# Kernel optimization log

Hardware: AMD Instinct MI355X
Metric: run time of the kernel (lower is better)

The kernel has to match this reference:

```python
import jax, jax.numpy as jnp
import numpy as np

D_MODEL, D_STATE, D_CONV, EXPAND = 1024, 16, 4, 2
D_INNER = EXPAND * D_MODEL            # 2048
DT_RANK = (D_MODEL + 15) // 16        # 64 (mamba 'auto')
B, L = 2, 2048
EPS = 1e-5


def setup_inputs() -> dict:
    key = jax.random.key(0)
    ks = jax.random.split(key, 12)
    s = lambda k, shape, sc=0.02: jax.random.normal(k, shape, dtype=jnp.float32) * sc
    return {
        "x": jax.random.normal(ks[0], (B, L, D_MODEL), dtype=jnp.float32),
        "ln_w": jnp.ones((D_MODEL,), jnp.float32),
        "ln_b": jnp.zeros((D_MODEL,), jnp.float32),
        "W_in": s(ks[1], (2 * D_INNER, D_MODEL)),
        "conv_w": s(ks[2], (D_INNER, D_CONV), 0.2),
        "conv_b": jnp.zeros((D_INNER,), jnp.float32),
        "W_xproj": s(ks[3], (DT_RANK + 2 * D_STATE, D_INNER)),
        "W_dt": s(ks[4], (D_INNER, DT_RANK), 0.1),
        "b_dt": jax.random.uniform(ks[5], (D_INNER,), jnp.float32, -4.0, -2.0),  # softplus(b)~dt_min
        "A_log": jnp.log(jnp.broadcast_to(jnp.arange(1, D_STATE + 1, dtype=jnp.float32), (D_INNER, D_STATE))),
        "D": jnp.ones((D_INNER,), jnp.float32),
        "W_out": s(ks[6], (D_MODEL, D_INNER)),
    }


def _mamba_forward(x, ln_w, ln_b, W_in, conv_w, conv_b, W_xproj, W_dt, b_dt, A_log, D, W_out):
    # Pre-norm LayerNorm
    mu = jnp.mean(x, axis=-1, keepdims=True)
    var = jnp.mean(jnp.square(x - mu), axis=-1, keepdims=True)
    xn = (x - mu) * jax.lax.rsqrt(var + EPS) * ln_w + ln_b

    # in_proj -> [B, L, 2*d_inner]; split into x-branch and gate z
    xz = jnp.einsum("bld,ed->ble", xn, W_in)
    u, z = jnp.split(xz, 2, axis=-1)

    # causal depthwise conv1d over L, kernel width D_CONV
    u_pad = jnp.pad(u, ((0, 0), (D_CONV - 1, 0), (0, 0)))
    uc = conv_b[None, None, :]
    for k in range(D_CONV):
        uc = uc + u_pad[:, k:k + L, :] * conv_w[:, k]
    u = jax.nn.silu(uc)  # [B, L, d_inner]

    # input-dependent dt, B, C
    dbl = jnp.einsum("bld,ed->ble", u, W_xproj)
    dt_r = dbl[..., :DT_RANK]
    Bm = dbl[..., DT_RANK:DT_RANK + D_STATE]          # [B, L, n]
    Cm = dbl[..., DT_RANK + D_STATE:]                 # [B, L, n]
    dt = jax.nn.softplus(jnp.einsum("blr,dr->bld", dt_r, W_dt) + b_dt)  # [B, L, d]

    A = -jnp.exp(A_log)  # [d, n]

    # selective scan over L; carry h: [B, d, n]
    def step(h, inp):
        dt_t, B_t, C_t, u_t = inp  # [B,d], [B,n], [B,n], [B,d]
        dA = jnp.exp(dt_t[:, :, None] * A[None])                 # [B, d, n]
        h = dA * h + (dt_t * u_t)[:, :, None] * B_t[:, None, :]  # [B, d, n]
        y_t = jnp.einsum("bdn,bn->bd", h, C_t)
        return h, y_t

    xs = (jnp.moveaxis(dt, 1, 0), jnp.moveaxis(Bm, 1, 0),
          jnp.moveaxis(Cm, 1, 0), jnp.moveaxis(u, 1, 0))
    h0 = jnp.zeros((x.shape[0], D_INNER, D_STATE), x.dtype)
    _, ys = jax.lax.scan(step, h0, xs)
    y = jnp.moveaxis(ys, 0, 1) + u * D  # [B, L, d_inner]

    y = y * jax.nn.silu(z)
    out = jnp.einsum("bld,ed->ble", y, W_out)
    return x + out


def reference(x, ln_w, ln_b, W_in, conv_w, conv_b, W_xproj, W_dt, b_dt, A_log, D, W_out):
    return _mamba_forward(x, ln_w, ln_b, W_in, conv_w, conv_b, W_xproj, W_dt, b_dt, A_log, D, W_out)
```

## Files before the change

kernel.cpp:

```cpp
#include <hip/hip_runtime.h>
#include <hip/hip_bf16.h>
#include <stdint.h>

typedef __hip_bfloat16 bf16;
typedef __attribute__((ext_vector_type(8))) short short8;
typedef __attribute__((ext_vector_type(4))) short short4v;
typedef __attribute__((ext_vector_type(4))) float floatx4;

#define D_MODEL 1024
#define D_STATE 16
#define D_INNER 2048
#define DT_RANK 64
#define BB 2
#define LL 2048
#define BL (BB * LL)
#define XZ_LD (2 * D_INNER)
#define DBL_LD (DT_RANK + 2 * D_STATE)
#define NCH 64
#define TCH (LL / NCH)

__device__ __forceinline__ bf16 f2b(float f) { return __float2bfloat16(f); }

__device__ __forceinline__ float fsig(float v)  { return __fdividef(1.f, 1.f + __expf(-v)); }
__device__ __forceinline__ float fsoftp(float v){ return fmaxf(v, 0.f) + __logf(1.f + __expf(-fabsf(v))); }

__device__ __forceinline__ void gload16(const void* g, void* l) {
    __builtin_amdgcn_global_load_lds(
        (const __attribute__((address_space(1))) uint32_t*)(uintptr_t)g,
        (__attribute__((address_space(3))) uint32_t*)(uintptr_t)l,
        16, 0, 0);
}

#define S0 (4096 * 1024)
#define S1 (128 * 2048)
#define S2 (2048 * 64)
#define S3 (1024 * 2048)
#define S4 (BL * DBL_LD)
#define WCVT_TOT (S0 + S1 + S2 + S3 + S4)

__global__ __launch_bounds__(256) void prep_kernel(
    const float* __restrict__ x, const float* __restrict__ w,
    const float* __restrict__ b, bf16* __restrict__ xnb,
    const float* __restrict__ Win, const float* __restrict__ Wx,
    const float* __restrict__ Wdt, const float* __restrict__ Wout,
    bf16* __restrict__ win_bf, bf16* __restrict__ wx_bf,
    bf16* __restrict__ wdt_bf, bf16* __restrict__ wout_bf,
    float* __restrict__ dbl)
{
    __shared__ float s1[256], s2[256];
    const int tid = threadIdx.x;
    if (blockIdx.x < BL) {
        const int row = blockIdx.x;
        const float* xr = x + (size_t)row * D_MODEL;
        float v[4], sum = 0.f, sq = 0.f;
#pragma unroll
        for (int i = 0; i < 4; ++i) {
            v[i] = xr[tid + 256 * i];
            sum += v[i];
            sq  += v[i] * v[i];
        }
        s1[tid] = sum; s2[tid] = sq;
        __syncthreads();
        for (int s = 128; s > 0; s >>= 1) {
            if (tid < s) { s1[tid] += s1[tid + s]; s2[tid] += s2[tid + s]; }
            __syncthreads();
        }
        const float mu  = s1[0] * (1.f / D_MODEL);
        const float var = s2[0] * (1.f / D_MODEL) - mu * mu;
        const float rs  = rsqrtf(var + 1e-5f);
#pragma unroll
        for (int i = 0; i < 4; ++i) {
            const int c = tid + 256 * i;
            xnb[(size_t)row * D_MODEL + c] = f2b((v[i] - mu) * rs * w[c] + b[c]);
        }
    } else {
        int id = (blockIdx.x - BL) * 256 + tid;
        if (id < S0) { win_bf[id] = f2b(Win[id]); return; }
        id -= S0;
        if (id < S1) { wx_bf[id] = (id < 96 * 2048) ? f2b(Wx[id]) : f2b(0.f); return; }
        id -= S1;
        if (id < S2) { wdt_bf[id] = f2b(Wdt[id]); return; }
        id -= S2;
        if (id < S3) { wout_bf[id] = f2b(Wout[id]); return; }
        id -= S3;
        dbl[id] = 0.f;
    }
}

#define GTM 128
#define GTN 128
#define GTK 32

template <int EPI>
__global__ __launch_bounds__(256) void gemm_t(
    const bf16* __restrict__ A, int lda,
    const bf16* __restrict__ B, int ldb,
    float* __restrict__ C, int ldc,
    int N, int K,
    const float* __restrict__ bias,
    bf16* __restrict__ C2)
{
    __shared__ short As[GTM * GTK];
    __shared__ short Bs[GTN * GTK];
    const int tid  = threadIdx.x;
    const int lane = tid & 63;
    const int wave = tid >> 6;
    const int wm = (wave & 1) * 64;
    const int wn = (wave >> 1) * 64;
    const int bm = blockIdx.y * GTM;
    const int bn = blockIdx.x * GTN;
    const int kbase = blockIdx.z * K;

    floatx4 acc[4][4];
#pragma unroll
    for (int i = 0; i < 4; ++i)
#pragma unroll
        for (int j = 0; j < 4; ++j) acc[i][j] = (floatx4){0.f, 0.f, 0.f, 0.f};

    const int srow = wave * 16 + (lane >> 2);
    const int scol = (lane & 3) * 8;
    const int fm = lane & 15;
    const int q  = lane >> 4;

    for (int k0 = 0; k0 < K; k0 += GTK) {
#pragma unroll
        for (int r = 0; r < 2; ++r) {
            const int m = r * 64 + srow;
            gload16(A + (size_t)(bm + m) * lda + kbase + k0 + scol,
                    As + m * GTK + scol);
            gload16(B + (size_t)(bn + m) * ldb + kbase + k0 + scol,
                    Bs + m * GTK + scol);
        }
        __syncthreads();

        short8 af[4], bfr[4];
#pragma unroll
        for (int i = 0; i < 4; ++i)
            af[i] = *(short8*)&As[(wm + i * 16 + fm) * GTK + q * 8];
#pragma unroll
        for (int j = 0; j < 4; ++j)
            bfr[j] = *(short8*)&Bs[(wn + j * 16 + fm) * GTK + q * 8];
#pragma unroll
        for (int i = 0; i < 4; ++i)
#pragma unroll
            for (int j = 0; j < 4; ++j)
                acc[i][j] = __builtin_amdgcn_mfma_f32_16x16x32_bf16(
                    af[i], bfr[j], acc[i][j], 0, 0, 0);
        __syncthreads();
    }

    const int col = lane & 15;
    const int rq  = (lane >> 4) * 4;
#pragma unroll
    for (int i = 0; i < 4; ++i) {
#pragma unroll
        for (int j = 0; j < 4; ++j) {
#pragma unroll
            for (int r = 0; r < 4; ++r) {
                const int gm = bm + wm + i * 16 + rq + r;
                const int gn = bn + wn + j * 16 + col;
                if (gn >= N) continue;
                float v = acc[i][j][r];
                if constexpr (EPI == 3) {
                    atomicAdd(&C[(size_t)gm * ldc + gn], v);
                } else if constexpr (EPI == 4) {
                    if (gn < D_INNER) C[(size_t)gm * ldc + gn] = v;
                    else C2[(size_t)gm * (size_t)D_INNER + (gn - D_INNER)] = f2b(v);
                } else {
                    C2[(size_t)gm * ldc + gn] = f2b(fsoftp(v + bias[gn]));
                }
            }
        }
    }
}

#define PNT (D_MODEL / 64)

__global__ __launch_bounds__(512, 2) void gemm256_uz(
    const bf16* __restrict__ A,
    const bf16* __restrict__ B,
    float* __restrict__ U,
    bf16* __restrict__ Z)
{
    __shared__ __attribute__((aligned(16))) short lds[65536];
    const int t    = threadIdx.x;
    const int lane = t & 63;
    const int wid  = t >> 6;
    const int wm   = wid >> 2;
    const int wn   = wid & 3;
    const int fm   = lane & 15;
    const int q    = lane >> 4;

    const int lin = (int)blockIdx.x;
    const int nid = (lin & 7) * 32 + (lin >> 3);
    const int bm  = (nid >> 4) * 256;
    const int bn  = (nid & 15) * 256;

    const int sg   = (((t & 7) ^ ((t >> 3) & 7)) << 3);
    const int ldst = t * 8;
    const short* Agp = (const short*)A + (size_t)(bm + (t >> 3)) * D_MODEL + sg;
    const short* Bgp = (const short*)B + (size_t)(bn + (t >> 3)) * D_MODEL + sg;

#define STG(g, lb) do { \
        gload16((g),                           &lds[(lb) + ldst]);        \
        gload16((g) + (size_t)64 * D_MODEL,    &lds[(lb) + 4096 + ldst]); \
    } while (0)

    const int ss0 = ((q ^ (fm & 7)) << 3);
    const int ss1 = (((4 + q) ^ (fm & 7)) << 3);
    const int aro = fm * 64;
    const int bro = ((wn & 1) * 64 + fm) * 64;

    floatx4 acc[8][4];
#pragma unroll
    for (int i = 0; i < 8; ++i)
#pragma unroll
        for (int j = 0; j < 4; ++j) acc[i][j] = (floatx4){0.f, 0.f, 0.f, 0.f};

    STG(Agp, 0);
    STG(Agp + (size_t)128 * D_MODEL, 8192);
    STG(Bgp, 32768);
    STG(Bgp + (size_t)128 * D_MODEL, 32768 + 8192);

    for (int kt = 0; kt < PNT; ++kt) {
        const int d = kt & 1;
        if (kt + 1 < PNT) {
            const int kn = (kt + 1) * 64;
            const int nb = (d ^ 1) * 16384;
            STG(Agp + kn,                         nb);
            STG(Agp + (size_t)128 * D_MODEL + kn, nb + 8192);
            STG(Bgp + kn,                         32768 + nb);
            STG(Bgp + (size_t)128 * D_MODEL + kn, 32768 + nb + 8192);
            asm volatile("s_waitcnt vmcnt(8)" ::: "memory");
        } else {
            asm volatile("s_waitcnt vmcnt(0)" ::: "memory");
        }
        __builtin_amdgcn_s_barrier();

        const short* Ab = &lds[d * 16384 + wm * 8192];
        const short* Bb = &lds[32768 + d * 16384 + (wn >> 1) * 8192];

        short8 bfr[4][2];
#pragma unroll
        for (int cf = 0; cf < 4; ++cf) {
            bfr[cf][0] = *(const short8*)(Bb + bro + cf * 1024 + ss0);
            bfr[cf][1] = *(const short8*)(Bb + bro + cf * 1024 + ss1);
        }

#pragma unroll
        for (int qd = 0; qd < 4; ++qd) {
            short8 af[2][2];
#pragma unroll
            for (int i = 0; i < 2; ++i) {
                af[i][0] = *(const short8*)(Ab + (qd * 2 + i) * 1024 + aro + ss0);
                af[i][1] = *(const short8*)(Ab + (qd * 2 + i) * 1024 + aro + ss1);
            }
            __builtin_amdgcn_s_barrier();
            __builtin_amdgcn_s_setprio(1);
#pragma unroll
            for (int i = 0; i < 2; ++i)
#pragma unroll
                for (int cf = 0; cf < 4; ++cf) {
                    acc[qd * 2 + i][cf] = __builtin_amdgcn_mfma_f32_16x16x32_bf16(
                        af[i][0], bfr[cf][0], acc[qd * 2 + i][cf], 0, 0, 0);
                    acc[qd * 2 + i][cf] = __builtin_amdgcn_mfma_f32_16x16x32_bf16(
                        af[i][1], bfr[cf][1], acc[qd * 2 + i][cf], 0, 0, 0);
                }
            __builtin_amdgcn_s_setprio(0);
            __builtin_amdgcn_s_barrier();
        }
    }
#undef STG

    const int gm0 = bm + wm * 128 + q * 4;
    const int gn0 = bn + wn * 64 + fm;
    if (bn < D_INNER) {
#pragma unroll
        for (int rf = 0; rf < 8; ++rf)
#pragma unroll
            for (int cf = 0; cf < 4; ++cf)
#pragma unroll
                for (int r = 0; r < 4; ++r)
                    U[(size_t)(gm0 + rf * 16 + r) * D_INNER + gn0 + cf * 16] =
                        acc[rf][cf][r];
    } else {
#pragma unroll
        for (int rf = 0; rf < 8; ++rf)
#pragma unroll
            for (int cf = 0; cf < 4; ++cf)
#pragma unroll
                for (int r = 0; r < 4; ++r)
                    Z[(size_t)(gm0 + rf * 16 + r) * D_INNER + gn0 + cf * 16 - D_INNER] =
                        f2b(acc[rf][cf][r]);
    }
}

#define ONT (D_INNER / 64)

__global__ __launch_bounds__(512, 2) void gemm_out8(
    const bf16* __restrict__ A,
    const bf16* __restrict__ B,
    const float* __restrict__ resid,
    float* __restrict__ C)
{
    __shared__ __attribute__((aligned(16))) short lds[32768];
    const int t    = threadIdx.x;
    const int lane = t & 63;
    const int wid  = t >> 6;
    const int wm   = wid >> 2;
    const int wn   = wid & 3;
    const int fm   = lane & 15;
    const int q    = lane >> 4;

    const int lin = (int)blockIdx.x;
    const int nid = (lin & 7) * 32 + (lin >> 3);
    const int bm  = (nid >> 3) * 128;
    const int bn  = (nid & 7) * 128;

    const int sg   = (((t & 7) ^ ((t >> 3) & 7)) << 3);
    const int ldst = t * 8;
    const short* Agp = (const short*)A + (size_t)(bm + (t >> 3)) * D_INNER + sg;
    const short* Bgp = (const short*)B + (size_t)(bn + (t >> 3)) * D_INNER + sg;

#define OSTG(g, lb) do { \
        gload16((g),                        &lds[(lb) + ldst]);        \
        gload16((g) + (size_t)64 * D_INNER, &lds[(lb) + 4096 + ldst]); \
    } while (0)

    const int ss0 = ((q ^ (fm & 7)) << 3);
    const int ss1 = (((4 + q) ^ (fm & 7)) << 3);
    const int fro = fm * 64;

    floatx4 acc[4][2];
#pragma unroll
    for (int i = 0; i < 4; ++i)
#pragma unroll
        for (int j = 0; j < 2; ++j) acc[i][j] = (floatx4){0.f, 0.f, 0.f, 0.f};

    OSTG(Agp, 0);
    OSTG(Bgp, 16384);

    for (int kt = 0; kt < ONT; ++kt) {
        const int d = kt & 1;
        if (kt + 1 < ONT) {
            const int kn = (kt + 1) * 64;
            const int nb = (d ^ 1) * 8192;
            OSTG(Agp + kn, nb);
            OSTG(Bgp + kn, 16384 + nb);
            asm volatile("s_waitcnt vmcnt(4)" ::: "memory");
        } else {
            asm volatile("s_waitcnt vmcnt(0)" ::: "memory");
        }
        __builtin_amdgcn_s_barrier();

        const short* Ab = &lds[d * 8192 + wm * 4096];
        const short* Bb = &lds[16384 + d * 8192 + wn * 2048];

        short8 bfr[2][2];
#pragma unroll
        for (int cf = 0; cf < 2; ++cf) {
            bfr[cf][0] = *(const short8*)(Bb + cf * 1024 + fro + ss0);
            bfr[cf][1] = *(const short8*)(Bb + cf * 1024 + fro + ss1);
        }

#pragma unroll
        for (int qd = 0; qd < 2; ++qd) {
            short8 af[2][2];
#pragma unroll
            for (int i = 0; i < 2; ++i) {
                af[i][0] = *(const short8*)(Ab + (qd * 2 + i) * 1024 + fro + ss0);
                af[i][1] = *(const short8*)(Ab + (qd * 2 + i) * 1024 + fro + ss1);
            }
            __builtin_amdgcn_s_barrier();
            __builtin_amdgcn_s_setprio(1);
#pragma unroll
            for (int i = 0; i < 2; ++i)
#pragma unroll
                for (int cf = 0; cf < 2; ++cf) {
                    acc[qd * 2 + i][cf] = __builtin_amdgcn_mfma_f32_16x16x32_bf16(
                        af[i][0], bfr[cf][0], acc[qd * 2 + i][cf], 0, 0, 0);
                    acc[qd * 2 + i][cf] = __builtin_amdgcn_mfma_f32_16x16x32_bf16(
                        af[i][1], bfr[cf][1], acc[qd * 2 + i][cf], 0, 0, 0);
                }
            __builtin_amdgcn_s_setprio(0);
            __builtin_amdgcn_s_barrier();
        }
    }
#undef OSTG

    const int gm0 = bm + wm * 64 + q * 4;
    const int gn0 = bn + wn * 32 + fm;
#pragma unroll
    for (int i = 0; i < 4; ++i)
#pragma unroll
        for (int cf = 0; cf < 2; ++cf)
#pragma unroll
            for (int r = 0; r < 4; ++r) {
                const size_t idx = (size_t)(gm0 + i * 16 + r) * D_MODEL + gn0 + cf * 16;
                C[idx] = acc[i][cf][r] + resid[idx];
            }
}

#define CCH 128
#define CTC (LL / CCH)

__global__ __launch_bounds__(256) void conv_v2(
    const float* __restrict__ uraw, const float* __restrict__ cw,
    const float* __restrict__ cb, bf16* __restrict__ ucb)
{
    const int blk = blockIdx.x;
    const int c  = blk & (CCH - 1);
    const int dg = (blk >> 7) & 1;
    const int b  = blk >> 8;
    const int d4 = dg * 1024 + threadIdx.x * 4;
    float w0[4], w1[4], w2[4], w3[4], bias[4];
#pragma unroll
    for (int j = 0; j < 4; ++j) {
        bias[j] = cb[d4 + j];
        w0[j] = cw[(d4 + j) * 4 + 0];
        w1[j] = cw[(d4 + j) * 4 + 1];
        w2[j] = cw[(d4 + j) * 4 + 2];
        w3[j] = cw[(d4 + j) * 4 + 3];
    }
    const size_t base = ((size_t)b * LL + (size_t)c * CTC) * D_INNER + d4;
    floatx4 x0 = {0.f, 0.f, 0.f, 0.f}, x1 = x0, x2 = x0;
    if (c > 0) {
        x0 = *(const floatx4*)(uraw + base - 3 * (size_t)D_INNER);
        x1 = *(const floatx4*)(uraw + base - 2 * (size_t)D_INNER);
        x2 = *(const floatx4*)(uraw + base - 1 * (size_t)D_INNER);
    }
#pragma unroll
    for (int tt = 0; tt < CTC; ++tt) {
        const floatx4 x3 = *(const floatx4*)(uraw + base + (size_t)tt * D_INNER);
        short4v o;
#pragma unroll
        for (int j = 0; j < 4; ++j) {
            float a = bias[j] + x0[j] * w0[j] + x1[j] * w1[j]
                              + x2[j] * w2[j] + x3[j] * w3[j];
            a = a * fsig(a);
            bf16 h = f2b(a);
            unsigned short us;
            __builtin_memcpy(&us, &h, 2);
            o[j] = (short)us;
        }
        *(short4v*)(ucb + base + (size_t)tt * D_INNER) = o;
        x0 = x1; x1 = x2; x2 = x3;
    }
}

__global__ __launch_bounds__(256) void cvt_dtr(
    const float* __restrict__ dbl, bf16* __restrict__ dtr_bf)
{
    const int id = blockIdx.x * 256 + threadIdx.x;
    const int m = id >> 6, r = id & 63;
    dtr_bf[id] = f2b(dbl[(size_t)m * DBL_LD + r]);
}

__global__ __launch_bounds__(256) void scan_p1(
    const bf16* __restrict__ uc, const bf16* __restrict__ dtb,
    const float* __restrict__ dbl, const float* __restrict__ A_log,
    float* __restrict__ Psum, float* __restrict__ Hloc)
{
    const int blk = blockIdx.x;
    const int d = (blk & 7) * 256 + threadIdx.x;
    const int c = (blk >> 3) & (NCH - 1);
    const int b = blk >> 9;
    float A[D_STATE], h[D_STATE];
    bool lin = true;
#pragma unroll
    for (int n = 0; n < D_STATE; ++n) {
        A[n] = -__expf(A_log[d * D_STATE + n]);
        lin = lin && (fabsf(A[n] + (float)(n + 1)) < 1e-3f);
        h[n] = 0.f;
    }
    const size_t row0 = (size_t)b * LL + c * TCH;
    const bf16* dtp = dtb + row0 * D_INNER + d;
    const bf16* up  = uc  + row0 * D_INNER + d;
    const float* Bp = dbl + row0 * DBL_LD + DT_RANK;
    float S = 0.f;
    if (lin) {
        for (int t = 0; t < TCH; ++t) {
            const float dtv = (float)dtp[(size_t)t * D_INNER];
            const float uv  = (float)up[(size_t)t * D_INNER];
            const float du  = dtv * uv;
            S += dtv;
            const float e1 = __expf(-dtv);
            float dA = 1.f;
#pragma unroll
            for (int n = 0; n < D_STATE; ++n) {
                dA *= e1;
                h[n] = dA * h[n] + du * Bp[(size_t)t * DBL_LD + n];
            }
        }
    } else {
        for (int t = 0; t < TCH; ++t) {
            const float dtv = (float)dtp[(size_t)t * D_INNER];
            const float uv  = (float)up[(size_t)t * D_INNER];
            const float du  = dtv * uv;
            S += dtv;
#pragma unroll
            for (int n = 0; n < D_STATE; ++n)
                h[n] = __expf(dtv * A[n]) * h[n] + du * Bp[(size_t)t * DBL_LD + n];
        }
    }
    const size_t o = (((size_t)b * NCH + c) * D_INNER + d) * D_STATE;
    if (lin) {
        const float E1 = __expf(-S);
        float P = 1.f;
#pragma unroll
        for (int n = 0; n < D_STATE; ++n) {
            P *= E1;
            Psum[o + n] = P;
            Hloc[o + n] = h[n];
        }
    } else {
#pragma unroll
        for (int n = 0; n < D_STATE; ++n) {
            Psum[o + n] = __expf(S * A[n]);
            Hloc[o + n] = h[n];
        }
    }
}

__global__ __launch_bounds__(256) void scan_p2(
    float* __restrict__ Psum, const float* __restrict__ Hloc)
{
    const int id = blockIdx.x * 256 + threadIdx.x;
    const int dn = id & (D_INNER * D_STATE - 1);
    const int b  = id >> 15;
    float h = 0.f;
    for (int c = 0; c < NCH; ++c) {
        const size_t o = ((size_t)(b * NCH + c) * D_INNER * D_STATE) + dn;
        const float P  = Psum[o];
        const float hl = Hloc[o];
        Psum[o] = h;
        h = P * h + hl;
    }
}

__global__ __launch_bounds__(256) void scan_p3b(
    bf16* __restrict__ ucy, const bf16* __restrict__ dtb,
    const float* __restrict__ dbl, const float* __restrict__ A_log,
    const float* __restrict__ Dw, const float* __restrict__ Hin,
    const bf16* __restrict__ zbf)
{
    const int blk = blockIdx.x;
    const int d = (blk & 7) * 256 + threadIdx.x;
    const int c = (blk >> 3) & (NCH - 1);
    const int b = blk >> 9;
    float A[D_STATE], h[D_STATE];
    const size_t o = (((size_t)b * NCH + c) * D_INNER + d) * D_STATE;
    bool lin = true;
#pragma unroll
    for (int n = 0; n < D_STATE; ++n) {
        A[n] = -__expf(A_log[d * D_STATE + n]);
        lin = lin && (fabsf(A[n] + (float)(n + 1)) < 1e-3f);
        h[n] = Hin[o + n];
    }
    const float Dd = Dw[d];
    const size_t row0 = (size_t)b * LL + c * TCH;
    const bf16* dtp = dtb + row0 * D_INNER + d;
    bf16*       uyp = ucy + row0 * D_INNER + d;
    const float* BCp = dbl + row0 * DBL_LD;
    const bf16* zp   = zbf + row0 * D_INNER + d;
    if (lin) {
        for (int t = 0; t < TCH; ++t) {
            const float dtv = (float)dtp[(size_t)t * D_INNER];
            const float uv  = (float)uyp[(size_t)t * D_INNER];
            const float du  = dtv * uv;
            float acc = uv * Dd;
            const float* Brow = BCp + (size_t)t * DBL_LD + DT_RANK;
            const float* Crow = Brow + D_STATE;
            const float e1 = __expf(-dtv);
            float dA = 1.f;
#pragma unroll
            for (int n = 0; n < D_STATE; ++n) {
                dA *= e1;
                h[n] = dA * h[n] + du * Brow[n];
                acc += h[n] * Crow[n];
            }
            const float zv = (float)zp[(size_t)t * D_INNER];
            uyp[(size_t)t * D_INNER] = f2b(acc * zv * fsig(zv));
        }
    } else {
        for (int t = 0; t < TCH; ++t) {
            const float dtv = (float)dtp[(size_t)t * D_INNER];
            const float uv  = (float)uyp[(size_t)t * D_INNER];
            const float du  = dtv * uv;
            float acc = uv * Dd;
            const float* Brow = BCp + (size_t)t * DBL_LD + DT_RANK;
            const float* Crow = Brow + D_STATE;
#pragma unroll
            for (int n = 0; n < D_STATE; ++n) {
                h[n] = __expf(dtv * A[n]) * h[n] + du * Brow[n];
                acc += h[n] * Crow[n];
            }
            const float zv = (float)zp[(size_t)t * D_INNER];
            uyp[(size_t)t * D_INNER] = f2b(acc * zv * fsig(zv));
        }
    }
}

#define BM 128
#define BN 128
#define BK 8

__global__ __launch_bounds__(256) void ln_kernel(
    const float* __restrict__ x, const float* __restrict__ w,
    const float* __restrict__ b, float* __restrict__ xnf)
{
    __shared__ float s1[256], s2[256];
    const int row = blockIdx.x;
    const int tid = threadIdx.x;
    const float* xr = x + (size_t)row * D_MODEL;
    float v[4], sum = 0.f, sq = 0.f;
#pragma unroll
    for (int i = 0; i < 4; ++i) {
        v[i] = xr[tid + 256 * i];
        sum += v[i];
        sq  += v[i] * v[i];
    }
    s1[tid] = sum; s2[tid] = sq;
    __syncthreads();
    for (int s = 128; s > 0; s >>= 1) {
        if (tid < s) { s1[tid] += s1[tid + s]; s2[tid] += s2[tid + s]; }
        __syncthreads();
    }
    const float mu  = s1[0] * (1.f / D_MODEL);
    const float var = s2[0] * (1.f / D_MODEL) - mu * mu;
    const float rs  = rsqrtf(var + 1e-5f);
#pragma unroll
    for (int i = 0; i < 4; ++i) {
        const int c = tid + 256 * i;
        xnf[(size_t)row * D_MODEL + c] = (v[i] - mu) * rs * w[c] + b[c];
    }
}

__global__ __launch_bounds__(256) void gemm_bt(
    const float* __restrict__ A, int lda,
    const float* __restrict__ Bw,
    float* __restrict__ C, int ldc,
    int M, int N, int K, int epi,
    const float* __restrict__ bias,
    const float* __restrict__ resid)
{
    __shared__ float As[BK][BM + 1];
    __shared__ float Bs[BK][BN + 1];
    const int tx = threadIdx.x, ty = threadIdx.y;
    const int tid = ty * 16 + tx;
    const int bm = blockIdx.y * BM, bn = blockIdx.x * BN;
    float acc[8][8];
#pragma unroll
    for (int i = 0; i < 8; ++i)
#pragma unroll
        for (int j = 0; j < 8; ++j) acc[i][j] = 0.f;
    for (int k0 = 0; k0 < K; k0 += BK) {
#pragma unroll
        for (int i = tid; i < BM * BK; i += 256) {
            const int m = i / BK, kk = i % BK;
            As[kk][m] = A[(size_t)(bm + m) * lda + (k0 + kk)];
        }
#pragma unroll
        for (int i = tid; i < BN * BK; i += 256) {
            const int n = i / BK, kk = i % BK;
            const int gn = bn + n;
            Bs[kk][n] = (gn < N) ? Bw[(size_t)gn * K + (k0 + kk)] : 0.f;
        }
        __syncthreads();
#pragma unroll
        for (int kk = 0; kk < BK; ++kk) {
            float av[8], bv[8];
#pragma unroll
            for (int i = 0; i < 8; ++i) av[i] = As[kk][ty * 8 + i];
#pragma unroll
            for (int j = 0; j < 8; ++j) bv[j] = Bs[kk][tx * 8 + j];
#pragma unroll
            for (int i = 0; i < 8; ++i)
#pragma unroll
                for (int j = 0; j < 8; ++j) acc[i][j] += av[i] * bv[j];
        }
        __syncthreads();
    }
#pragma unroll
    for (int i = 0; i < 8; ++i) {
        const int gm = bm + ty * 8 + i;
#pragma unroll
        for (int j = 0; j < 8; ++j) {
            const int gn = bn + tx * 8 + j;
            if (gn >= N) continue;
            float v = acc[i][j];
            if (epi == 1) {
                v += bias[gn];
                v = fmaxf(v, 0.f) + log1pf(expf(-fabsf(v)));
            } else if (epi == 2) {
                v += resid[(size_t)gm * ldc + gn];
            }
            C[(size_t)gm * ldc + gn] = v;
        }
    }
}

__global__ __launch_bounds__(256) void conv_silu_kernel(
    float* __restrict__ xz, const float* __restrict__ cw,
    const float* __restrict__ cb)
{
    const int idx = blockIdx.x * 256 + threadIdx.x;
    const int b = idx >> 11, d = idx & (D_INNER - 1);
    const float w0 = cw[d * 4 + 0], w1 = cw[d * 4 + 1];
    const float w2 = cw[d * 4 + 2], w3 = cw[d * 4 + 3];
    const float bias = cb[d];
    float* u = xz + (size_t)b * LL * XZ_LD + d;
    float x0 = 0.f, x1 = 0.f, x2 = 0.f;
    for (int t = 0; t < LL; ++t) {
        const float x3 = u[(size_t)t * XZ_LD];
        const float c = bias + x0 * w0 + x1 * w1 + x2 * w2 + x3 * w3;
        u[(size_t)t * XZ_LD] = c / (1.f + expf(-c));
        x0 = x1; x1 = x2; x2 = x3;
    }
}

__global__ __launch_bounds__(256) void scan_kernel(
    float* __restrict__ xz, const float* __restrict__ dtb,
    const float* __restrict__ dbl,
    const float* __restrict__ A_log, const float* __restrict__ Dw)
{
    const int idx = blockIdx.x * 256 + threadIdx.x;
    const int b = idx >> 11, d = idx & (D_INNER - 1);
    float A[D_STATE], h[D_STATE];
#pragma unroll
    for (int n = 0; n < D_STATE; ++n) {
        A[n] = -expf(A_log[d * D_STATE + n]);
        h[n] = 0.f;
    }
    const float Dd = Dw[d];
    const float* dtp  = dtb + (size_t)b * LL * D_INNER + d;
    float*       up   = xz  + (size_t)b * LL * XZ_LD + d;
    const float* dblp = dbl + (size_t)b * LL * DBL_LD;
    for (int t = 0; t < LL; ++t) {
        const float dtv = dtp[(size_t)t * D_INNER];
        const float uv  = up[(size_t)t * XZ_LD];
        const float zv  = up[(size_t)t * XZ_LD + D_INNER];
        const float* Brow = dblp + (size_t)t * DBL_LD + DT_RANK;
        const float* Crow = Brow + D_STATE;
        const float du = dtv * uv;
        float acc = uv * Dd;
#pragma unroll
        for (int n = 0; n < D_STATE; ++n) {
            const float dA = expf(dtv * A[n]);
            h[n] = dA * h[n] + du * Brow[n];
            acc += h[n] * Crow[n];
        }
        const float sz = zv / (1.f + expf(-zv));
        up[(size_t)t * XZ_LD] = acc * sz;
    }
}

extern "C" void kernel_launch(void* const* d_in, const int* in_sizes, int n_in,
                              void* d_out, int out_size, void* d_ws, size_t ws_size,
                              hipStream_t stream)
{
    const float* x       = (const float*)d_in[0];
    const float* ln_w    = (const float*)d_in[1];
    const float* ln_b    = (const float*)d_in[2];
    const float* W_in    = (const float*)d_in[3];
    const float* conv_w  = (const float*)d_in[4];
    const float* conv_b  = (const float*)d_in[5];
    const float* W_xproj = (const float*)d_in[6];
    const float* W_dt    = (const float*)d_in[7];
    const float* b_dt    = (const float*)d_in[8];
    const float* A_log   = (const float*)d_in[9];
    const float* Dw      = (const float*)d_in[10];
    const float* W_out   = (const float*)d_in[11];
    float* out = (float*)d_out;

    float* wsf     = (float*)d_ws;
    bf16*  dtb_bf  = (bf16*)wsf;
    float* uraw    = wsf + 4194304;
    bf16*  zbf     = (bf16*)(wsf + 12582912);
    float* Psum    = wsf + 16777216;
    float* Hloc    = wsf + 20971520;
    float* dbl     = wsf + 25165824;
    bf16*  ucy     = (bf16*)(wsf + 25559040);
    bf16*  xn_bf   = (bf16*)(wsf + 29753344);
    bf16*  win_bf  = (bf16*)(wsf + 31850496);
    bf16*  wx_bf   = (bf16*)(wsf + 33947648);
    bf16*  wdt_bf  = (bf16*)(wsf + 34078720);
    bf16*  wout_bf = (bf16*)(wsf + 34144256);
    bf16*  dtr_bf  = (bf16*)(wsf + 35192832);
    const size_t need_big = (size_t)35323904 * sizeof(float);

    if (ws_size >= need_big) {
        prep_kernel<<<BL + WCVT_TOT / 256, 256, 0, stream>>>(
            x, ln_w, ln_b, xn_bf,
            W_in, W_xproj, W_dt, W_out, win_bf, wx_bf, wdt_bf, wout_bf, dbl);
        gemm256_uz<<<dim3(256), 512, 0, stream>>>(xn_bf, win_bf, uraw, zbf);
        conv_v2<<<BB * 2 * CCH, 256, 0, stream>>>(uraw, conv_w, conv_b, ucy);
        gemm_t<3><<<dim3(1, BL / GTM, 8), 256, 0, stream>>>(
            ucy, D_INNER, wx_bf, D_INNER, dbl, DBL_LD,
            DBL_LD, D_INNER / 8, nullptr, nullptr);
        cvt_dtr<<<BL * DT_RANK / 256, 256, 0, stream>>>(dbl, dtr_bf);
        gemm_t<5><<<dim3(D_INNER / GTN, BL / GTM, 1), 256, 0, stream>>>(
            dtr_bf, DT_RANK, wdt_bf, DT_RANK, nullptr, D_INNER,
            D_INNER, DT_RANK, b_dt, dtb_bf);
        scan_p1<<<BB * NCH * 8, 256, 0, stream>>>(
            ucy, dtb_bf, dbl, A_log, Psum, Hloc);
        scan_p2<<<BB * D_INNER * D_STATE / 256, 256, 0, stream>>>(Psum, Hloc);
        scan_p3b<<<BB * NCH * 8, 256, 0, stream>>>(
            ucy, dtb_bf, dbl, A_log, Dw, Psum, zbf);
        gemm_out8<<<dim3(256), 512, 0, stream>>>(ucy, wout_bf, x, out);
    } else {
        float* fdtb = wsf;
        float* fxn  = fdtb;
        float* fxz  = fdtb + (size_t)BL * D_INNER;
        float* fdbl = fxz + (size_t)BL * XZ_LD;
        ln_kernel<<<BL, 256, 0, stream>>>(x, ln_w, ln_b, fxn);
        dim3 blk(16, 16);
        gemm_bt<<<dim3(XZ_LD / BN, BL / BM), blk, 0, stream>>>(
            fxn, D_MODEL, W_in, fxz, XZ_LD, BL, XZ_LD, D_MODEL, 0, nullptr, nullptr);
        conv_silu_kernel<<<(BB * D_INNER) / 256, 256, 0, stream>>>(fxz, conv_w, conv_b);
        gemm_bt<<<dim3(1, BL / BM), blk, 0, stream>>>(
            fxz, XZ_LD, W_xproj, fdbl, DBL_LD, BL, DBL_LD, D_INNER, 0, nullptr, nullptr);
        gemm_bt<<<dim3(D_INNER / BN, BL / BM), blk, 0, stream>>>(
            fdbl, DBL_LD, W_dt, fdtb, D_INNER, BL, D_INNER, DT_RANK, 1, b_dt, nullptr);
        scan_kernel<<<(BB * D_INNER) / 256, 256, 0, stream>>>(fxz, fdtb, fdbl, A_log, Dw);
        gemm_bt<<<dim3(D_MODEL / BN, BL / BM), blk, 0, stream>>>(
            fxz, XZ_LD, W_out, out, D_MODEL, BL, D_MODEL, D_INNER, 2, nullptr, x);
    }
}
```

Baseline: 284.5 us.

## Shrink in_proj GEMM tiles to 128 and replace split-K atomics with partial-sum reduction

The in_proj GEMM moves from 256x256 tiles (256 blocks) to 128x128 tiles (1024 blocks) with half the LDS, giving more blocks to spread across CUs at the cost of less per-tile reuse. The x_proj split-K GEMM now writes per-split partial sums into a scratch buffer (reusing the uraw region) instead of doing atomicAdd into dbl. A new reduction kernel sums the 8 partials and writes both dbl and the bf16 dt_rank slice, which replaces the separate cvt_dtr kernel. This removes atomic contention and the pre-zeroing dependency on dbl, but adds an extra pass over the partial buffer.

```diff
diff --git a/kernel.cpp b/kernel.cpp
--- a/kernel.cpp
+++ b/kernel.cpp
@@ -161,11 +161,8 @@
                 const int gn = bn + wn + j * 16 + col;
                 if (gn >= N) continue;
                 float v = acc[i][j][r];
-                if constexpr (EPI == 3) {
-                    atomicAdd(&C[(size_t)gm * ldc + gn], v);
-                } else if constexpr (EPI == 4) {
-                    if (gn < D_INNER) C[(size_t)gm * ldc + gn] = v;
-                    else C2[(size_t)gm * (size_t)D_INNER + (gn - D_INNER)] = f2b(v);
+                if constexpr (EPI == 6) {
+                    C[((size_t)blockIdx.z * BL + gm) * 128 + gn] = v;
                 } else {
                     C2[(size_t)gm * ldc + gn] = f2b(fsoftp(v + bias[gn]));
                 }
@@ -174,15 +171,29 @@
     }
 }
 
-#define PNT (D_MODEL / 64)
-
-__global__ __launch_bounds__(512, 2) void gemm256_uz(
+__global__ __launch_bounds__(256) void red_dbl(
+    const float* __restrict__ P, float* __restrict__ dbl,
+    bf16* __restrict__ dtr_bf)
+{
+    const int id = blockIdx.x * 256 + threadIdx.x;
+    const int n = id & 127, m = id >> 7;
+    if (n >= DBL_LD) return;
+    float s = 0.f;
+#pragma unroll
+    for (int k = 0; k < 8; ++k) s += P[(size_t)k * BL * 128 + id];
+    dbl[(size_t)m * DBL_LD + n] = s;
+    if (n < DT_RANK) dtr_bf[(size_t)m * DT_RANK + n] = f2b(s);
+}
+
+#define GNT (D_MODEL / 64)
+
+__global__ __launch_bounds__(512, 2) void gemm128_uz(
     const bf16* __restrict__ A,
     const bf16* __restrict__ B,
     float* __restrict__ U,
     bf16* __restrict__ Z)
 {
-    __shared__ __attribute__((aligned(16))) short lds[65536];
+    __shared__ __attribute__((aligned(16))) short lds[32768];
     const int t    = threadIdx.x;
     const int lane = t & 63;
     const int wid  = t >> 6;
@@ -192,75 +203,70 @@
     const int q    = lane >> 4;
 
     const int lin = (int)blockIdx.x;
-    const int nid = (lin & 7) * 32 + (lin >> 3);
-    const int bm  = (nid >> 4) * 256;
-    const int bn  = (nid & 15) * 256;
+    const int nid = (lin & 7) * 128 + (lin >> 3);
+    const int bm  = (nid >> 5) * 128;
+    const int bn  = (nid & 31) * 128;
 
     const int sg   = (((t & 7) ^ ((t >> 3) & 7)) << 3);
     const int ldst = t * 8;
     const short* Agp = (const short*)A + (size_t)(bm + (t >> 3)) * D_MODEL + sg;
     const short* Bgp = (const short*)B + (size_t)(bn + (t >> 3)) * D_MODEL + sg;
 
-#define STG(g, lb) do { \
-        gload16((g),                           &lds[(lb) + ldst]);        \
-        gload16((g) + (size_t)64 * D_MODEL,    &lds[(lb) + 4096 + ldst]); \
+#define GSTG(g, lb) do { \
+        gload16((g),                        &lds[(lb) + ldst]);        \
+        gload16((g) + (size_t)64 * D_MODEL, &lds[(lb) + 4096 + ldst]); \
     } while (0)
 
     const int ss0 = ((q ^ (fm & 7)) << 3);
     const int ss1 = (((4 + q) ^ (fm & 7)) << 3);
-    const int aro = fm * 64;
-    const int bro = ((wn & 1) * 64 + fm) * 64;
-
-    floatx4 acc[8][4];
-#pragma unroll
-    for (int i = 0; i < 8; ++i)
-#pragma unroll
-        for (int j = 0; j < 4; ++j) acc[i][j] = (floatx4){0.f, 0.f, 0.f, 0.f};
-
-    STG(Agp, 0);
-    STG(Agp + (size_t)128 * D_MODEL, 8192);
-    STG(Bgp, 32768);
-    STG(Bgp + (size_t)128 * D_MODEL, 32768 + 8192);
-
-    for (int kt = 0; kt < PNT; ++kt) {
+    const int fro = fm * 64;
+
+    floatx4 acc[4][2];
+#pragma unroll
+    for (int i = 0; i < 4; ++i)
+#pragma unroll
+        for (int j = 0; j < 2; ++j) acc[i][j] = (floatx4){0.f, 0.f, 0.f, 0.f};
+
+    GSTG(Agp, 0);
+    GSTG(Bgp, 16384);
+
+    for (int kt = 0; kt < GNT; ++kt) {
         const int d = kt & 1;
-        if (kt + 1 < PNT) {
+        if (kt + 1 < GNT) {
             const int kn = (kt + 1) * 64;
-            const int nb = (d ^ 1) * 16384;
-            STG(Agp + kn,                         nb);
-            STG(Agp + (size_t)128 * D_MODEL + kn, nb + 8192);
-            STG(Bgp + kn,                         32768 + nb);
-            STG(Bgp + (size_t)128 * D_MODEL + kn, 32768 + nb + 8192);
-            asm volatile("s_waitcnt vmcnt(8)" ::: "memory");
+            const int nb = (d ^ 1) * 8192;
+            GSTG(Agp + kn, nb);
+            GSTG(Bgp + kn, 16384 + nb);
+            asm volatile("s_waitcnt vmcnt(4)" ::: "memory");
         } else {
             asm volatile("s_waitcnt vmcnt(0)" ::: "memory");
         }
         __builtin_amdgcn_s_barrier();
 
-        const short* Ab = &lds[d * 16384 + wm * 8192];
-        const short* Bb = &lds[32768 + d * 16384 + (wn >> 1) * 8192];
-
-        short8 bfr[4][2];
-#pragma unroll
-        for (int cf = 0; cf < 4; ++cf) {
-            bfr[cf][0] = *(const short8*)(Bb + bro + cf * 1024 + ss0);
-            bfr[cf][1] = *(const short8*)(Bb + bro + cf * 1024 + ss1);
-        }
-
-#pragma unroll
-        for (int qd = 0; qd < 4; ++qd) {
+        const short* Ab = &lds[d * 8192 + wm * 4096];
+        const short* Bb = &lds[16384 + d * 8192 + wn * 2048];
+
+        short8 bfr[2][2];
+#pragma unroll
+        for (int cf = 0; cf < 2; ++cf) {
+            bfr[cf][0] = *(const short8*)(Bb + cf * 1024 + fro + ss0);
+            bfr[cf][1] = *(const short8*)(Bb + cf * 1024 + fro + ss1);
+        }
+
+#pragma unroll
+        for (int qd = 0; qd < 2; ++qd) {
             short8 af[2][2];
 #pragma unroll
             for (int i = 0; i < 2; ++i) {
-                af[i][0] = *(const short8*)(Ab + (qd * 2 + i) * 1024 + aro + ss0);
-                af[i][1] = *(const short8*)(Ab + (qd * 2 + i) * 1024 + aro + ss1);
+                af[i][0] = *(const short8*)(Ab + (qd * 2 + i) * 1024 + fro + ss0);
+                af[i][1] = *(const short8*)(Ab + (qd * 2 + i) * 1024 + fro + ss1);
             }
             __builtin_amdgcn_s_barrier();
             __builtin_amdgcn_s_setprio(1);
 #pragma unroll
             for (int i = 0; i < 2; ++i)
 #pragma unroll
-                for (int cf = 0; cf < 4; ++cf) {
+                for (int cf = 0; cf < 2; ++cf) {
                     acc[qd * 2 + i][cf] = __builtin_amdgcn_mfma_f32_16x16x32_bf16(
                         af[i][0], bfr[cf][0], acc[qd * 2 + i][cf], 0, 0, 0);
                     acc[qd * 2 + i][cf] = __builtin_amdgcn_mfma_f32_16x16x32_bf16(
@@ -270,28 +276,28 @@
             __builtin_amdgcn_s_barrier();
         }
     }
-#undef STG
-
-    const int gm0 = bm + wm * 128 + q * 4;
-    const int gn0 = bn + wn * 64 + fm;
+#undef GSTG
+
+    const int gm0 = bm + wm * 64 + q * 4;
+    const int gn0 = bn + wn * 32 + fm;
     if (bn < D_INNER) {
 #pragma unroll
-        for (int rf = 0; rf < 8; ++rf)
-#pragma unroll
-            for (int cf = 0; cf < 4; ++cf)
+        for (int i = 0; i < 4; ++i)
+#pragma unroll
+            for (int cf = 0; cf < 2; ++cf)
 #pragma unroll
                 for (int r = 0; r < 4; ++r)
-                    U[(size_t)(gm0 + rf * 16 + r) * D_INNER + gn0 + cf * 16] =
-                        acc[rf][cf][r];
+                    U[(size_t)(gm0 + i * 16 + r) * D_INNER + gn0 + cf * 16] =
+                        acc[i][cf][r];
     } else {
 #pragma unroll
-        for (int rf = 0; rf < 8; ++rf)
-#pragma unroll
-            for (int cf = 0; cf < 4; ++cf)
+        for (int i = 0; i < 4; ++i)
+#pragma unroll
+            for (int cf = 0; cf < 2; ++cf)
 #pragma unroll
                 for (int r = 0; r < 4; ++r)
-                    Z[(size_t)(gm0 + rf * 16 + r) * D_INNER + gn0 + cf * 16 - D_INNER] =
-                        f2b(acc[rf][cf][r]);
+                    Z[(size_t)(gm0 + i * 16 + r) * D_INNER + gn0 + cf * 16 - D_INNER] =
+                        f2b(acc[i][cf][r]);
     }
 }
 
@@ -446,14 +452,6 @@
         *(short4v*)(ucb + base + (size_t)tt * D_INNER) = o;
         x0 = x1; x1 = x2; x2 = x3;
     }
-}
-
-__global__ __launch_bounds__(256) void cvt_dtr(
-    const float* __restrict__ dbl, bf16* __restrict__ dtr_bf)
-{
-    const int id = blockIdx.x * 256 + threadIdx.x;
-    const int m = id >> 6, r = id & 63;
-    dtr_bf[id] = f2b(dbl[(size_t)m * DBL_LD + r]);
 }
 
 __global__ __launch_bounds__(256) void scan_p1(
@@ -793,12 +791,12 @@
         prep_kernel<<<BL + WCVT_TOT / 256, 256, 0, stream>>>(
             x, ln_w, ln_b, xn_bf,
             W_in, W_xproj, W_dt, W_out, win_bf, wx_bf, wdt_bf, wout_bf, dbl);
-        gemm256_uz<<<dim3(256), 512, 0, stream>>>(xn_bf, win_bf, uraw, zbf);
+        gemm128_uz<<<dim3(1024), 512, 0, stream>>>(xn_bf, win_bf, uraw, zbf);
         conv_v2<<<BB * 2 * CCH, 256, 0, stream>>>(uraw, conv_w, conv_b, ucy);
-        gemm_t<3><<<dim3(1, BL / GTM, 8), 256, 0, stream>>>(
-            ucy, D_INNER, wx_bf, D_INNER, dbl, DBL_LD,
-            DBL_LD, D_INNER / 8, nullptr, nullptr);
-        cvt_dtr<<<BL * DT_RANK / 256, 256, 0, stream>>>(dbl, dtr_bf);
+        gemm_t<6><<<dim3(1, BL / GTM, 8), 256, 0, stream>>>(
+            ucy, D_INNER, wx_bf, D_INNER, uraw, 128,
+            128, D_INNER / 8, nullptr, nullptr);
+        red_dbl<<<BL * 128 / 256, 256, 0, stream>>>(uraw, dbl, dtr_bf);
         gemm_t<5><<<dim3(D_INNER / GTN, BL / GTM, 1), 256, 0, stream>>>(
             dtr_bf, DT_RANK, wdt_bf, DT_RANK, nullptr, D_INNER,
             D_INNER, DT_RANK, b_dt, dtb_bf);
```

Result: slower. 291.6 us (+2.5%).
